# Kernel tuning notes

Measured on AMD Instinct MI355X. Metric: run time of the kernel, lower is better.

The kernel has to match this reference:

```python
import jax, jax.numpy as jnp
import numpy as np
from jax import lax


def setup_inputs() -> dict:
    key = jax.random.key(0)
    ks = jax.random.split(key, 8)
    b, l, d_model = 2, 1024, 768
    expand, d_state, d_conv = 2, 16, 4
    d_inner = d_model * expand            # 1536
    dt_rank = -(-d_model // 16)           # ceil(768/16) = 48
    x = jax.random.normal(ks[0], (b, l, d_model), jnp.float32)
    W_in = jax.random.normal(ks[1], (d_model, 2 * d_inner), jnp.float32) * 0.02
    conv_w = jax.random.normal(ks[2], (d_inner, 1, d_conv), jnp.float32) * 0.1
    conv_b = jnp.zeros((d_inner,), jnp.float32)
    W_x = jax.random.normal(ks[3], (d_inner, dt_rank + 2 * d_state), jnp.float32) * 0.02
    W_dt = jax.random.normal(ks[4], (dt_rank, d_inner), jnp.float32) * 0.02
    b_dt = jax.random.normal(ks[5], (d_inner,), jnp.float32) * 0.02
    # A_log = log(1..d_state) broadcast over d_inner, as in the module init
    A_log = jnp.broadcast_to(jnp.log(jnp.arange(1, d_state + 1, dtype=jnp.float32)), (d_inner, d_state)).copy()
    D = jnp.ones((d_inner,), jnp.float32)
    W_out = jax.random.normal(ks[6], (d_inner, d_model), jnp.float32) * 0.02
    return {"x": x, "W_in": W_in, "conv_w": conv_w, "conv_b": conv_b, "W_x": W_x,
            "W_dt": W_dt, "b_dt": b_dt, "A_log": A_log, "D": D, "W_out": W_out}


def _silu(v):
    return v * jax.nn.sigmoid(v)


def reference(x, W_in, conv_w, conv_b, W_x, W_dt, b_dt, A_log, D, W_out):
    b, l, d_model = x.shape
    d_inner, _, d_conv = conv_w.shape
    dt_rank = W_dt.shape[0]
    n = A_log.shape[1]

    # in_proj and split into x / res paths
    x_and_res = x @ W_in                              # (b, l, 2*d_inner)
    xi, res = jnp.split(x_and_res, 2, axis=-1)

    # depthwise causal conv1d (torch pads d_conv-1 both sides then slices [:l])
    xc = jnp.transpose(xi, (0, 2, 1))                 # (b, d_inner, l)
    xc = lax.conv_general_dilated(
        xc, conv_w, window_strides=(1,), padding=[(d_conv - 1, 0)],
        dimension_numbers=("NCH", "OIH", "NCH"), feature_group_count=d_inner)
    xc = xc + conv_b[None, :, None]
    u = _silu(jnp.transpose(xc, (0, 2, 1)))           # (b, l, d_inner)

    # SSM parameters (input-dependent)
    A = -jnp.exp(A_log.astype(jnp.float32))           # (d_inner, n)
    x_dbl = u @ W_x                                   # (b, l, dt_rank + 2n)
    delta = x_dbl[..., :dt_rank]
    B = x_dbl[..., dt_rank:dt_rank + n]               # (b, l, n)
    C = x_dbl[..., dt_rank + n:]                      # (b, l, n)
    delta = jax.nn.softplus(delta @ W_dt + b_dt)      # (b, l, d_inner)

    # discretize
    deltaA = jnp.exp(delta[..., None] * A)            # (b, l, d_inner, n)
    deltaB_u = delta[..., None] * B[:, :, None, :] * u[..., None]  # (b, l, d_inner, n)

    # parallel associative scan over l: h_t = deltaA_t * h_{t-1} + deltaB_u_t
    def combine(c1, c2):
        a1, b1 = c1
        a2, b2 = c2
        return (a1 * a2, a2 * b1 + b2)

    _, hs = lax.associative_scan(combine, (deltaA, deltaB_u), axis=1)  # (b, l, d_inner, n)

    y = jnp.einsum("bldn,bln->bld", hs, C) + u * D    # (b, l, d_inner)
    y = y * _silu(res)
    out = y @ W_out                                   # (b, l, d_model)
    return out
```

## Files before the change

### kernel.cpp

```cpp
#include <hip/hip_runtime.h>
#include <math.h>

#define DI 1536
#define DM 768
#define NSTATE 16
#define DTRANK 48
#define LSEQ 1024
#define NBATCH 2
#define MROWS (NBATCH*LSEQ)
#define NXR 3072
#define NCHUNK 32
#define CLEN 32
#define SCB 128

typedef __attribute__((ext_vector_type(4))) float f32x4;
typedef __attribute__((ext_vector_type(8))) short s16x8;
typedef __attribute__((ext_vector_type(4))) unsigned int u32x4;

__device__ __forceinline__ unsigned short f2bf(float f) {
  unsigned int x = __builtin_bit_cast(unsigned int, f);
  return (unsigned short)((x + 0x7fffu + ((x >> 16) & 1u)) >> 16);
}

__global__ __launch_bounds__(256) void convert_bf16_kernel(
    const float* __restrict__ in, unsigned short* __restrict__ out, long n)
{
  long i = ((long)blockIdx.x * 256 + threadIdx.x) * 8;
  if (i >= n) return;
  f32x4 v0 = *(const f32x4*)&in[i];
  f32x4 v1 = *(const f32x4*)&in[i + 4];
  unsigned short o[8];
  #pragma unroll
  for (int j = 0; j < 4; ++j) { o[j] = f2bf(v0[j]); o[4 + j] = f2bf(v1[j]); }
  *(u32x4*)&out[i] = *(u32x4*)o;
}

__global__ __launch_bounds__(256) void transpose_bf16_kernel(
    const float* __restrict__ in, unsigned short* __restrict__ out, int R, int C)
{
  __shared__ float t[32][33];
  int ctile = blockIdx.x * 32, rtile = blockIdx.y * 32;
  int tx = threadIdx.x & 31, ty = threadIdx.x >> 5;
  #pragma unroll
  for (int i = 0; i < 4; ++i) {
    int r = ty + i * 8;
    t[r][tx] = in[(long)(rtile + r) * C + ctile + tx];
  }
  __syncthreads();
  #pragma unroll
  for (int i = 0; i < 4; ++i) {
    int cc = ty + i * 8;
    out[(long)(ctile + cc) * R + rtile + tx] = f2bf(t[tx][cc]);
  }
}

__global__ __launch_bounds__(256) void transpose_bf16_guard(
    const float* __restrict__ in, unsigned short* __restrict__ out, int R, int C)
{
  __shared__ float t[32][33];
  int ctile = blockIdx.x * 32, rtile = blockIdx.y * 32;
  int tx = threadIdx.x & 31, ty = threadIdx.x >> 5;
  #pragma unroll
  for (int i = 0; i < 4; ++i) {
    int r = ty + i * 8;
    if (rtile + r < R && ctile + tx < C)
      t[r][tx] = in[(long)(rtile + r) * C + ctile + tx];
  }
  __syncthreads();
  #pragma unroll
  for (int i = 0; i < 4; ++i) {
    int cc = ty + i * 8;
    if (ctile + cc < C && rtile + tx < R)
      out[(long)(ctile + cc) * R + rtile + tx] = f2bf(t[tx][cc]);
  }
}

template<int FM, int FN>
__global__ __launch_bounds__(256) void gemm_bf16(
    const unsigned short* __restrict__ A,
    const unsigned short* __restrict__ BT,
    float* __restrict__ C, int M, int N, int K)
{
  constexpr int BM = 32 * FM, BN = 32 * FN;
  __shared__ unsigned short Ap[BM * 32];
  __shared__ unsigned short Bp[BN * 32];
  const int tid = threadIdx.x;
  const int lane = tid & 63, wave = tid >> 6;
  const int wr = wave >> 1, wc = wave & 1;
  const int lg = lane >> 4, lr = lane & 15;
  const int m0 = blockIdx.y * BM, n0 = blockIdx.x * BN;
  f32x4 acc[FM][FN] = {};
  const int rs = tid >> 2;
  const int kg = tid & 3;
  for (int k0 = 0; k0 < K; k0 += 32) {
    #pragma unroll
    for (int p = 0; p < BM / 64; ++p) {
      int r = p * 64 + rs;
      u32x4 v = *(const u32x4*)&A[(long)(m0 + r) * K + k0 + kg * 8];
      int slot = ((r >> 4) * 4 + kg) * 16 + (r & 15);
      *(u32x4*)&Ap[slot * 8] = v;
    }
    #pragma unroll
    for (int p = 0; p < BN / 64; ++p) {
      int r = p * 64 + rs;
      u32x4 v = *(const u32x4*)&BT[(long)(n0 + r) * K + k0 + kg * 8];
      int slot = ((r >> 4) * 4 + kg) * 16 + (r & 15);
      *(u32x4*)&Bp[slot * 8] = v;
    }
    __syncthreads();
    s16x8 af[FM], bfr[FN];
    #pragma unroll
    for (int m = 0; m < FM; ++m)
      af[m] = *(s16x8*)&Ap[(((wr * FM + m) * 4 + lg) * 16 + lr) * 8];
    #pragma unroll
    for (int n = 0; n < FN; ++n)
      bfr[n] = *(s16x8*)&Bp[(((wc * FN + n) * 4 + lg) * 16 + lr) * 8];
    #pragma unroll
    for (int m = 0; m < FM; ++m)
      #pragma unroll
      for (int n = 0; n < FN; ++n)
        acc[m][n] = __builtin_amdgcn_mfma_f32_16x16x32_bf16(af[m], bfr[n], acc[m][n], 0, 0, 0);
    __syncthreads();
  }
  #pragma unroll
  for (int m = 0; m < FM; ++m)
    #pragma unroll
    for (int n = 0; n < FN; ++n)
      #pragma unroll
      for (int r = 0; r < 4; ++r) {
        int row = m0 + wr * 16 * FM + m * 16 + lg * 4 + r;
        int col = n0 + wc * 16 * FN + n * 16 + lr;
        C[(long)row * N + col] = acc[m][n][r];
      }
}

__global__ __launch_bounds__(256) void conv_silu_kernel(
    const float* __restrict__ xr,
    const float* __restrict__ conv_w,
    const float* __restrict__ conv_b,
    float* __restrict__ u,
    unsigned short* __restrict__ u_bf)
{
  int idx = blockIdx.x * 256 + threadIdx.x;
  if (idx >= MROWS * DI) return;
  int c = idx % DI;
  int bm = idx / DI;
  int t = bm % LSEQ;
  int b = bm / LSEQ;
  float w0 = conv_w[c * 4 + 0], w1 = conv_w[c * 4 + 1];
  float w2 = conv_w[c * 4 + 2], w3 = conv_w[c * 4 + 3];
  const float* xc = xr + (long)b * LSEQ * NXR + c;
  float acc = conv_b[c];
  if (t >= 3) acc = fmaf(xc[(long)(t - 3) * NXR], w0, acc);
  if (t >= 2) acc = fmaf(xc[(long)(t - 2) * NXR], w1, acc);
  if (t >= 1) acc = fmaf(xc[(long)(t - 1) * NXR], w2, acc);
  acc = fmaf(xc[(long)t * NXR], w3, acc);
  float s = acc / (1.f + __expf(-acc));
  u[idx] = s;
  u_bf[idx] = f2bf(s);
}

__global__ __launch_bounds__(256) void xdbl_mfma(
    const unsigned short* __restrict__ u_bf,
    const unsigned short* __restrict__ WxT,
    float* __restrict__ xdbl)
{
  const int tid = threadIdx.x;
  const int lane = tid & 63, wave = tid >> 6;
  const int lg = lane >> 4, lr = lane & 15;
  const int m0 = blockIdx.x * 16;
  f32x4 acc[5] = {};
  const int kbase = wave * (DI / 4);
  #pragma unroll
  for (int kk = 0; kk < DI / 4; kk += 32) {
    int k0 = kbase + kk;
    s16x8 af = *(const s16x8*)&u_bf[(long)(m0 + lr) * DI + k0 + lg * 8];
    #pragma unroll
    for (int n = 0; n < 5; ++n) {
      s16x8 bfr = *(const s16x8*)&WxT[(long)(n * 16 + lr) * DI + k0 + lg * 8];
      acc[n] = __builtin_amdgcn_mfma_f32_16x16x32_bf16(af, bfr, acc[n], 0, 0, 0);
    }
  }
  __shared__ float red[4][16][80];
  #pragma unroll
  for (int n = 0; n < 5; ++n)
    #pragma unroll
    for (int r = 0; r < 4; ++r)
      red[wave][lg * 4 + r][n * 16 + lr] = acc[n][r];
  __syncthreads();
  for (int i = tid; i < 16 * 80; i += 256) {
    int row = i / 80, col = i % 80;
    float s = red[0][row][col] + red[1][row][col] + red[2][row][col] + red[3][row][col];
    xdbl[(long)(m0 + row) * 80 + col] = s;
  }
}

__global__ __launch_bounds__(256) void delta_kernel(
    const float* __restrict__ xdbl,
    const float* __restrict__ W_dt,
    const float* __restrict__ b_dt,
    float* __restrict__ delta)
{
  __shared__ float sx[DTRANK];
  int m = blockIdx.y;
  int c = blockIdx.x * 256 + threadIdx.x;
  if (threadIdx.x < DTRANK) sx[threadIdx.x] = xdbl[(long)m * 80 + threadIdx.x];
  __syncthreads();
  float acc = b_dt[c];
  #pragma unroll 8
  for (int r = 0; r < DTRANK; ++r)
    acc = fmaf(sx[r], W_dt[(long)r * DI + c], acc);
  float sp = (acc > 20.f) ? acc : log1pf(__expf(acc));
  delta[(long)m * DI + c] = sp;
}

__global__ __launch_bounds__(SCB) void scan_ph1(
    const float* __restrict__ delta,
    const float* __restrict__ xdbl,
    const float* __restrict__ u,
    const float* __restrict__ A_log,
    float* __restrict__ Aprod,
    float* __restrict__ Hend)
{
  const int b = blockIdx.z, chunk = blockIdx.y;
  const int tid = threadIdx.x;
  const int d = blockIdx.x * SCB + tid;
  const long mbase = (long)b * LSEQ + chunk * CLEN;
  __shared__ float sB[CLEN][NSTATE];
  for (int i = tid; i < CLEN * NSTATE; i += SCB) {
    int t = i >> 4, j = i & 15;
    sB[t][j] = xdbl[(mbase + t) * 80 + DTRANK + j];
  }
  __syncthreads();
  float a[NSTATE];
  #pragma unroll
  for (int n = 0; n < NSTATE; ++n)
    a[n] = -__expf(A_log[(long)d * NSTATE + n]);
  float h[NSTATE] = {};
  float Ap[NSTATE];
  #pragma unroll
  for (int n = 0; n < NSTATE; ++n) Ap[n] = 1.f;
  #pragma unroll 4
  for (int t = 0; t < CLEN; ++t) {
    long m = mbase + t;
    float dt = delta[m * DI + d];
    float uu = u[m * DI + d];
    float dtu = dt * uu;
    #pragma unroll
    for (int n = 0; n < NSTATE; ++n) {
      float dA = __expf(dt * a[n]);
      Ap[n] *= dA;
      h[n] = fmaf(dA, h[n], dtu * sB[t][n]);
    }
  }
  long o = (((long)b * NCHUNK + chunk) * DI + d) * NSTATE;
  #pragma unroll
  for (int q = 0; q < 4; ++q) {
    f32x4 va = { Ap[q*4+0], Ap[q*4+1], Ap[q*4+2], Ap[q*4+3] };
    f32x4 vh = { h[q*4+0], h[q*4+1], h[q*4+2], h[q*4+3] };
    *(f32x4*)&Aprod[o + q*4] = va;
    *(f32x4*)&Hend[o + q*4] = vh;
  }
}

__global__ __launch_bounds__(256) void scan_ph2(
    const float* __restrict__ Aprod,
    const float* __restrict__ Hend,
    float* __restrict__ Hstart)
{
  int idx = blockIdx.x * 256 + threadIdx.x;
  int b = idx / (DI * NSTATE);
  int r = idx % (DI * NSTATE);
  long o = (long)b * NCHUNK * DI * NSTATE + r;
  const long stride = (long)DI * NSTATE;
  float h = 0.f;
  #pragma unroll
  for (int c = 0; c < NCHUNK; ++c) {
    float Ap = Aprod[o + c * stride];
    float He = Hend[o + c * stride];
    Hstart[o + c * stride] = h;
    h = fmaf(Ap, h, He);
  }
}

__global__ __launch_bounds__(SCB) void scan_ph3(
    const float* __restrict__ delta,
    const float* __restrict__ xdbl,
    const float* __restrict__ u,
    const float* __restrict__ xr,
    const float* __restrict__ A_log,
    const float* __restrict__ Dp,
    const float* __restrict__ Hstart,
    unsigned short* __restrict__ yg)
{
  const int b = blockIdx.z, chunk = blockIdx.y;
  const int tid = threadIdx.x;
  const int d = blockIdx.x * SCB + tid;
  const long mbase = (long)b * LSEQ + chunk * CLEN;
  __shared__ float sB[CLEN][NSTATE], sC[CLEN][NSTATE];
  for (int i = tid; i < CLEN * NSTATE; i += SCB) {
    int t = i >> 4, j = i & 15;
    long mo = (mbase + t) * 80 + DTRANK + j;
    sB[t][j] = xdbl[mo];
    sC[t][j] = xdbl[mo + NSTATE];
  }
  __syncthreads();
  float a[NSTATE];
  #pragma unroll
  for (int n = 0; n < NSTATE; ++n)
    a[n] = -__expf(A_log[(long)d * NSTATE + n]);
  const float Dv = Dp[d];
  long o = (((long)b * NCHUNK + chunk) * DI + d) * NSTATE;
  float h[NSTATE];
  #pragma unroll
  for (int q = 0; q < 4; ++q) {
    f32x4 vh = *(const f32x4*)&Hstart[o + q*4];
    h[q*4+0] = vh[0]; h[q*4+1] = vh[1]; h[q*4+2] = vh[2]; h[q*4+3] = vh[3];
  }
  #pragma unroll 4
  for (int t = 0; t < CLEN; ++t) {
    long m = mbase + t;
    float dt = delta[m * DI + d];
    float uu = u[m * DI + d];
    float rr = xr[m * NXR + DI + d];
    float dtu = dt * uu;
    float p0 = 0.f, p1 = 0.f, p2 = 0.f, p3 = 0.f;
    #pragma unroll
    for (int q = 0; q < 4; ++q) {
      float dA0 = __expf(dt * a[q*4+0]);
      float dA1 = __expf(dt * a[q*4+1]);
      float dA2 = __expf(dt * a[q*4+2]);
      float dA3 = __expf(dt * a[q*4+3]);
      h[q*4+0] = fmaf(dA0, h[q*4+0], dtu * sB[t][q*4+0]);
      h[q*4+1] = fmaf(dA1, h[q*4+1], dtu * sB[t][q*4+1]);
      h[q*4+2] = fmaf(dA2, h[q*4+2], dtu * sB[t][q*4+2]);
      h[q*4+3] = fmaf(dA3, h[q*4+3], dtu * sB[t][q*4+3]);
    }
    #pragma unroll
    for (int n = 0; n < NSTATE; n += 4) {
      p0 = fmaf(h[n+0], sC[t][n+0], p0);
      p1 = fmaf(h[n+1], sC[t][n+1], p1);
      p2 = fmaf(h[n+2], sC[t][n+2], p2);
      p3 = fmaf(h[n+3], sC[t][n+3], p3);
    }
    float yv = (p0 + p1) + (p2 + p3) + uu * Dv;
    float gate = rr / (1.f + __expf(-rr));
    yg[m * DI + d] = f2bf(yv * gate);
  }
}

extern "C" void kernel_launch(void* const* d_in, const int* in_sizes, int n_in,
                              void* d_out, int out_size, void* d_ws, size_t ws_size,
                              hipStream_t stream)
{
  const float* x      = (const float*)d_in[0];
  const float* W_in   = (const float*)d_in[1];
  const float* conv_w = (const float*)d_in[2];
  const float* conv_b = (const float*)d_in[3];
  const float* W_x    = (const float*)d_in[4];
  const float* W_dt   = (const float*)d_in[5];
  const float* b_dt   = (const float*)d_in[6];
  const float* A_log  = (const float*)d_in[7];
  const float* Dp     = (const float*)d_in[8];
  const float* W_out  = (const float*)d_in[9];
  float* out = (float*)d_out;

  char* p = (char*)d_ws;
  float* xr     = (float*)(p + 0);
  float* u      = (float*)(p + 25165824);
  float* xdbl   = (float*)(p + 37748736);
  float* delta  = (float*)(p + 38404096);
  float* Aprod  = (float*)(p + 50987008);
  float* Hend   = (float*)(p + 57278464);
  unsigned short* yg    = (unsigned short*)(p + 63569920);
  unsigned short* WoutT = (unsigned short*)(p + 69861376);
  float* Hstart = (float*)(p + 72220672);
  unsigned short* x_bf = (unsigned short*)delta;
  unsigned short* WinT = (unsigned short*)Aprod;
  unsigned short* u_bf = (unsigned short*)Hend;
  unsigned short* WxT  = (unsigned short*)Hstart;

  convert_bf16_kernel<<<(MROWS * DM) / (256 * 8), 256, 0, stream>>>(x, x_bf, (long)MROWS * DM);
  transpose_bf16_kernel<<<dim3(NXR / 32, DM / 32), 256, 0, stream>>>(W_in, WinT, DM, NXR);
  transpose_bf16_kernel<<<dim3(DM / 32, DI / 32), 256, 0, stream>>>(W_out, WoutT, DI, DM);
  transpose_bf16_guard<<<dim3(3, DI / 32), 256, 0, stream>>>(W_x, WxT, DI, 80);
  gemm_bf16<4, 4><<<dim3(NXR / 128, MROWS / 128), 256, 0, stream>>>(
      x_bf, WinT, xr, MROWS, NXR, DM);
  conv_silu_kernel<<<(MROWS * DI + 255) / 256, 256, 0, stream>>>(xr, conv_w, conv_b, u, u_bf);
  xdbl_mfma<<<MROWS / 16, 256, 0, stream>>>(u_bf, WxT, xdbl);
  delta_kernel<<<dim3(DI / 256, MROWS), 256, 0, stream>>>(xdbl, W_dt, b_dt, delta);
  scan_ph1<<<dim3(DI / SCB, NCHUNK, NBATCH), SCB, 0, stream>>>(delta, xdbl, u, A_log, Aprod, Hend);
  scan_ph2<<<(NBATCH * DI * NSTATE) / 256, 256, 0, stream>>>(Aprod, Hend, Hstart);
  scan_ph3<<<dim3(DI / SCB, NCHUNK, NBATCH), SCB, 0, stream>>>(
      delta, xdbl, u, xr, A_log, Dp, Hstart, yg);
  gemm_bf16<2, 2><<<dim3(DM / 64, MROWS / 64), 256, 0, stream>>>(
      yg, WoutT, out, MROWS, DM, DI);
}
```

Before: 191.7 us.

## Use direct global-to-LDS loads in GEMM, batch delta rows, finer scan chunks

The GEMM tile staging now uses global_load_lds so data goes straight from global memory into shared memory without passing through registers, with the LDS layout matching the MFMA fragment order. The delta kernel now computes 16 rows per block, reusing each W_dt load across rows instead of re-reading it per row. The scan chunking moves from 32 chunks of 32 to 64 chunks of 16 for more parallelism in phases 1 and 3, at the cost of a longer serial phase 2 and larger Aprod/Hend buffers, so the workspace offsets are relaid.

```diff
diff --git a/kernel.cpp b/kernel.cpp
--- a/kernel.cpp
+++ b/kernel.cpp
@@ -9,9 +9,10 @@
 #define NBATCH 2
 #define MROWS (NBATCH*LSEQ)
 #define NXR 3072
-#define NCHUNK 32
-#define CLEN 32
+#define NCHUNK 64
+#define CLEN 16
 #define SCB 128
+#define DMP 16
 
 typedef __attribute__((ext_vector_type(4))) float f32x4;
 typedef __attribute__((ext_vector_type(8))) short s16x8;
@@ -20,6 +21,12 @@
 __device__ __forceinline__ unsigned short f2bf(float f) {
   unsigned int x = __builtin_bit_cast(unsigned int, f);
   return (unsigned short)((x + 0x7fffu + ((x >> 16) & 1u)) >> 16);
+}
+
+__device__ __forceinline__ void gload_lds16(const void* g, void* l) {
+  __builtin_amdgcn_global_load_lds(
+      (const __attribute__((address_space(1))) void*)g,
+      (__attribute__((address_space(3))) void*)l, 16, 0, 0);
 }
 
 __global__ __launch_bounds__(256) void convert_bf16_kernel(
@@ -82,6 +89,7 @@
     float* __restrict__ C, int M, int N, int K)
 {
   constexpr int BM = 32 * FM, BN = 32 * FN;
+  constexpr int TM = BM / 16, TN = BN / 16;
   __shared__ unsigned short Ap[BM * 32];
   __shared__ unsigned short Bp[BN * 32];
   const int tid = threadIdx.x;
@@ -90,22 +98,18 @@
   const int lg = lane >> 4, lr = lane & 15;
   const int m0 = blockIdx.y * BM, n0 = blockIdx.x * BN;
   f32x4 acc[FM][FN] = {};
-  const int rs = tid >> 2;
-  const int kg = tid & 3;
   for (int k0 = 0; k0 < K; k0 += 32) {
     #pragma unroll
-    for (int p = 0; p < BM / 64; ++p) {
-      int r = p * 64 + rs;
-      u32x4 v = *(const u32x4*)&A[(long)(m0 + r) * K + k0 + kg * 8];
-      int slot = ((r >> 4) * 4 + kg) * 16 + (r & 15);
-      *(u32x4*)&Ap[slot * 8] = v;
-    }
-    #pragma unroll
-    for (int p = 0; p < BN / 64; ++p) {
-      int r = p * 64 + rs;
-      u32x4 v = *(const u32x4*)&BT[(long)(n0 + r) * K + k0 + kg * 8];
-      int slot = ((r >> 4) * 4 + kg) * 16 + (r & 15);
-      *(u32x4*)&Bp[slot * 8] = v;
+    for (int p = 0; p < TM / 4; ++p) {
+      int tile = wave + p * 4;
+      gload_lds16(&A[(long)(m0 + tile * 16 + lr) * K + k0 + lg * 8],
+                  &Ap[tile * 512]);
+    }
+    #pragma unroll
+    for (int p = 0; p < TN / 4; ++p) {
+      int tile = wave + p * 4;
+      gload_lds16(&BT[(long)(n0 + tile * 16 + lr) * K + k0 + lg * 8],
+                  &Bp[tile * 512]);
     }
     __syncthreads();
     s16x8 af[FM], bfr[FN];
@@ -201,17 +205,31 @@
     const float* __restrict__ b_dt,
     float* __restrict__ delta)
 {
-  __shared__ float sx[DTRANK];
-  int m = blockIdx.y;
-  int c = blockIdx.x * 256 + threadIdx.x;
-  if (threadIdx.x < DTRANK) sx[threadIdx.x] = xdbl[(long)m * 80 + threadIdx.x];
-  __syncthreads();
-  float acc = b_dt[c];
-  #pragma unroll 8
-  for (int r = 0; r < DTRANK; ++r)
-    acc = fmaf(sx[r], W_dt[(long)r * DI + c], acc);
-  float sp = (acc > 20.f) ? acc : log1pf(__expf(acc));
-  delta[(long)m * DI + c] = sp;
+  __shared__ float sx[DMP][DTRANK];
+  const int tid = threadIdx.x;
+  const int c = blockIdx.x * 256 + tid;
+  const int m0 = blockIdx.y * DMP;
+  for (int i = tid; i < DMP * DTRANK; i += 256) {
+    int mm = i / DTRANK, r = i % DTRANK;
+    sx[mm][r] = xdbl[(long)(m0 + mm) * 80 + r];
+  }
+  __syncthreads();
+  float bias = b_dt[c];
+  float acc[DMP];
+  #pragma unroll
+  for (int mm = 0; mm < DMP; ++mm) acc[mm] = bias;
+  for (int r = 0; r < DTRANK; ++r) {
+    float wv = W_dt[(long)r * DI + c];
+    #pragma unroll
+    for (int mm = 0; mm < DMP; ++mm)
+      acc[mm] = fmaf(sx[mm][r], wv, acc[mm]);
+  }
+  #pragma unroll
+  for (int mm = 0; mm < DMP; ++mm) {
+    float v = acc[mm];
+    float sp = (v > 20.f) ? v : log1pf(__expf(v));
+    delta[(long)(m0 + mm) * DI + c] = sp;
+  }
 }
 
 __global__ __launch_bounds__(SCB) void scan_ph1(
@@ -274,7 +292,6 @@
   long o = (long)b * NCHUNK * DI * NSTATE + r;
   const long stride = (long)DI * NSTATE;
   float h = 0.f;
-  #pragma unroll
   for (int c = 0; c < NCHUNK; ++c) {
     float Ap = Aprod[o + c * stride];
     float He = Hend[o + c * stride];
@@ -371,10 +388,10 @@
   float* xdbl   = (float*)(p + 37748736);
   float* delta  = (float*)(p + 38404096);
   float* Aprod  = (float*)(p + 50987008);
-  float* Hend   = (float*)(p + 57278464);
-  unsigned short* yg    = (unsigned short*)(p + 63569920);
-  unsigned short* WoutT = (unsigned short*)(p + 69861376);
-  float* Hstart = (float*)(p + 72220672);
+  float* Hend   = (float*)(p + 63569920);
+  unsigned short* yg    = (unsigned short*)(p + 76152832);
+  unsigned short* WoutT = (unsigned short*)(p + 82444288);
+  float* Hstart = (float*)(p + 84803584);
   unsigned short* x_bf = (unsigned short*)delta;
   unsigned short* WinT = (unsigned short*)Aprod;
   unsigned short* u_bf = (unsigned short*)Hend;
@@ -388,7 +405,7 @@
       x_bf, WinT, xr, MROWS, NXR, DM);
   conv_silu_kernel<<<(MROWS * DI + 255) / 256, 256, 0, stream>>>(xr, conv_w, conv_b, u, u_bf);
   xdbl_mfma<<<MROWS / 16, 256, 0, stream>>>(u_bf, WxT, xdbl);
-  delta_kernel<<<dim3(DI / 256, MROWS), 256, 0, stream>>>(xdbl, W_dt, b_dt, delta);
+  delta_kernel<<<dim3(DI / 256, MROWS / DMP), 256, 0, stream>>>(xdbl, W_dt, b_dt, delta);
   scan_ph1<<<dim3(DI / SCB, NCHUNK, NBATCH), SCB, 0, stream>>>(delta, xdbl, u, A_log, Aprod, Hend);
   scan_ph2<<<(NBATCH * DI * NSTATE) / 256, 256, 0, stream>>>(Aprod, Hend, Hstart);
   scan_ph3<<<dim3(DI / SCB, NCHUNK, NBATCH), SCB, 0, stream>>>(
```

After: 176.2 us. 8.1% less time.
